# Performance work log

Hardware: AMD Instinct MI355X
Metric: run time of the kernel (lower is better)

The kernel has to match this reference:

```python
import jax, jax.numpy as jnp
import numpy as np

DIM = 512
HEADS = 8
LF, P = 32, 32
N = LF * P
LOC_DIM = 64  # loc_emd_dim == locf_dim == 64
SCALE = (DIM // HEADS) ** -0.5


def _position_matrix(boxes):
    # boxes: [N,4] x1y1x2y2 -> [N,N,4] relative geometry (relation-network style)
    x1, y1, x2, y2 = jnp.split(boxes, 4, axis=1)  # each [N,1]
    w = x2 - x1 + 1.0
    h = y2 - y1 + 1.0
    cx = 0.5 * (x1 + x2)
    cy = 0.5 * (y1 + y2)
    dx = jnp.log(jnp.maximum(jnp.abs((cx - cx.T) / w), 1e-3))
    dy = jnp.log(jnp.maximum(jnp.abs((cy - cy.T) / h), 1e-3))
    dw = jnp.log(w.T / w)
    dh = jnp.log(h.T / h)
    return jnp.stack([dx, dy, dw, dh], axis=-1)  # [N,N,4]


def _position_embedding(pos_mat, feat_dim=LOC_DIM, wave_length=1000.0):
    # pos_mat: [N,N,4] -> [N,N,feat_dim] sin/cos embedding
    nf = feat_dim // 8
    dim_mat = wave_length ** (jnp.arange(nf, dtype=jnp.float32) * (8.0 / feat_dim))  # [nf]
    div = pos_mat[..., None] * 100.0 / dim_mat  # [N,N,4,nf]
    emb = jnp.concatenate([jnp.sin(div), jnp.cos(div)], axis=-1)  # [N,N,4,2nf]
    return emb.reshape(pos_mat.shape[0], pos_mat.shape[1], feat_dim)


def setup_inputs() -> dict:
    key = jax.random.key(0)
    ks = jax.random.split(key, 8)
    x = jax.random.normal(ks[0], (1, N, DIM), jnp.float32)
    x_reg = jax.random.normal(ks[1], (1, N, DIM), jnp.float32)
    # valid boxes: x1y1x2y2 within a ~1000x600 frame
    cx = jax.random.uniform(ks[2], (LF, P, 1)) * 1000.0
    cy = jax.random.uniform(ks[3], (LF, P, 1)) * 600.0
    w = jax.random.uniform(ks[4], (LF, P, 1)) * 150.0 + 10.0
    h = jax.random.uniform(ks[5], (LF, P, 1)) * 150.0 + 10.0
    locs = jnp.concatenate([cx - w / 2, cy - h / 2, cx + w / 2, cy + h / 2], axis=-1)
    W_qkv = jax.random.normal(ks[6], (3 * DIM, DIM), jnp.float32) * 0.02
    W_loc = jax.random.normal(ks[7], (HEADS, LOC_DIM), jnp.float32) * 0.01  # 1x1 conv weight
    b_loc = jnp.zeros((HEADS,), jnp.float32)
    return {"x": x, "x_reg": x_reg, "locs": locs, "W_qkv": W_qkv, "W_loc": W_loc, "b_loc": b_loc}


def reference(x, x_reg, locs, W_qkv, W_loc, b_loc):
    B, n, C = x.shape
    boxes = locs.reshape(-1, 4)
    # location embedding -> 1x1 conv -> ReLU  (attn_lt: [H,N,N])
    pos_emb = _position_embedding(_position_matrix(boxes), LOC_DIM)  # [N,N,64]
    attn_lt = jax.nn.relu(jnp.einsum('nmf,hf->hnm', pos_emb, W_loc) + b_loc[:, None, None])
    # qkv projection (bias=False)
    qkv = (x @ W_qkv.T).reshape(B, n, 3, HEADS, C // HEADS)
    qkv = jnp.transpose(qkv, (2, 0, 3, 1, 4))  # [3,B,H,N,hd]
    q, k, v = qkv[0], qkv[1], qkv[2]
    attn = jnp.einsum('bhnd,bhmd->bhnm', q, k) * SCALE
    attn = attn + jnp.log(attn_lt + 1e-6)[None]  # loc_fuse_type == 'add'
    attn = jax.nn.softmax(attn, axis=-1)
    out = jnp.einsum('bhnm,bhmd->bhnd', attn, v)
    return jnp.transpose(out, (0, 2, 1, 3)).reshape(B, n, C)
```

## Files before the change

kernel.cpp:

```cpp
#include <hip/hip_runtime.h>
#include <hip/hip_bf16.h>


namespace {
constexpr int NN   = 1024;
constexpr int CDIM = 512;
constexpr int NH   = 8;
constexpr int HD   = 64;
constexpr int NOUT = 3 * CDIM;
constexpr int PROJ_BLOCKS = (NN / 64) * (NOUT / 64);
constexpr float QSCALE = 0.125f;

constexpr size_t QKBF_OFF_U16 = 0;
constexpr size_t VT_OFF_U16   = (size_t)2 * NH * NN * HD;
constexpr size_t XB_OFF_U16   = VT_OFF_U16 + (size_t)NH * HD * NN;
constexpr size_t WB_OFF_U16   = XB_OFF_U16 + (size_t)NN * CDIM;
constexpr size_t L_OFF_U16    = WB_OFF_U16 + (size_t)NOUT * CDIM;
constexpr size_t END_U16      = L_OFF_U16 + (size_t)NH * NN * NN;
constexpr size_t BF_OFF_F32   = END_U16 / 2;
constexpr size_t WR_OFF_F32   = BF_OFF_F32 + 6 * NN;
}

typedef __attribute__((ext_vector_type(8))) short short8v;
typedef __attribute__((ext_vector_type(4))) float f32x4;
typedef __attribute__((ext_vector_type(2))) float f32x2;

__device__ __forceinline__ unsigned short f2bf(float f) {
  union { float f; unsigned int u; } v; v.f = f;
  unsigned int u = v.u;
  u += 0x7fffu + ((u >> 16) & 1u);
  return (unsigned short)(u >> 16);
}
__device__ __forceinline__ float b2f(unsigned short u) {
  union { unsigned int u; float f; } v; v.u = ((unsigned int)u) << 16; return v.f;
}

__global__ __launch_bounds__(256) void k_cvt(const float* __restrict__ x,
                                             const float* __restrict__ wq,
                                             const float* __restrict__ locs,
                                             const float* __restrict__ wloc,
                                             const float* __restrict__ bloc,
                                             unsigned short* __restrict__ xb,
                                             unsigned short* __restrict__ wb,
                                             float* __restrict__ bf,
                                             float* __restrict__ wr) {
  constexpr int XTOT = NN * CDIM;
  constexpr int CVT_BLOCKS = 1280;
  int b = blockIdx.x;
  int tid = threadIdx.x;
  if (b < CVT_BLOCKS) {
    int idx = (b * 256 + tid) * 4;
    if (idx < XTOT) {
      float4 v = *reinterpret_cast<const float4*>(x + idx);
      ushort4 o;
      o.x = f2bf(v.x); o.y = f2bf(v.y); o.z = f2bf(v.z); o.w = f2bf(v.w);
      *reinterpret_cast<ushort4*>(xb + idx) = o;
    } else {
      int j = idx - XTOT;
      float4 v = *reinterpret_cast<const float4*>(wq + j);
      ushort4 o;
      o.x = f2bf(v.x); o.y = f2bf(v.y); o.z = f2bf(v.z); o.w = f2bf(v.w);
      *reinterpret_cast<ushort4*>(wb + j) = o;
    }
  } else {
    for (int i = tid; i < NN; i += 256) {
      float4 b4 = reinterpret_cast<const float4*>(locs)[i];
      float x1 = b4.x, y1 = b4.y, x2 = b4.z, y2 = b4.w;
      float w = x2 - x1 + 1.0f;
      float h = y2 - y1 + 1.0f;
      bf[0 * NN + i] = 0.5f * (x1 + x2);
      bf[1 * NN + i] = 0.5f * (y1 + y2);
      bf[2 * NN + i] = w;
      bf[3 * NN + i] = h;
      bf[4 * NN + i] = logf(w);
      bf[5 * NN + i] = logf(h);
    }
    for (int i = tid; i < 512; i += 256) {
      int hh = i & 7, c = (i >> 3) & 1, j = (i >> 4) & 3, t = i >> 6;
      wr[i] = wloc[hh * 64 + j * 16 + c * 8 + t];
    }
    if (tid < 8) wr[512 + tid] = bloc[tid];
  }
}

__global__ __launch_bounds__(256) void k_mid(const unsigned short* __restrict__ xb,
                                             const unsigned short* __restrict__ wb,
                                             unsigned short* __restrict__ qk_bf,
                                             unsigned short* __restrict__ vt,
                                             const float* __restrict__ bf,
                                             const float* __restrict__ wr,
                                             unsigned short* __restrict__ L) {
  __shared__ unsigned short A_lds[64][72];
  __shared__ unsigned short B_lds[64][72];
  int blk = blockIdx.x;
  int tid = threadIdx.x;

  if (blk >= PROJ_BLOCKS) {
    int blk2 = blk - PROJ_BLOCKS;
    int n = blk2 >> 2;
    int m = (blk2 & 3) * 256 + tid;
    const float* cx = bf;
    const float* cy = bf + NN;
    const float* bw = bf + 2 * NN;
    const float* bh = bf + 3 * NN;
    const float* lw = bf + 4 * NN;
    const float* lh = bf + 5 * NN;

    float cxn = cx[n], cyn = cy[n], wn = bw[n], hn = bh[n], lwn = lw[n], lhn = lh[n];
    float dx = __logf(fmaxf(fabsf((cxn - cx[m]) / wn), 1e-3f));
    float dy = __logf(fmaxf(fabsf((cyn - cy[m]) / hn), 1e-3f));
    float dw = lw[m] - lwn;
    float dh = lh[m] - lhn;
    float pos[4] = {dx, dy, dw, dh};

    const float ANG[8] = {100.0f, 42.169650342858224f, 17.78279410038923f,
                          7.498942093324559f, 3.1622776601683795f, 1.333521432163324f,
                          0.5623413251903491f, 0.23713737056616552f};

    f32x2 acc2[4] = {(f32x2){0.f, 0.f}, (f32x2){0.f, 0.f},
                     (f32x2){0.f, 0.f}, (f32x2){0.f, 0.f}};
#pragma unroll
    for (int t = 0; t < 8; ++t) {
#pragma unroll
      for (int j = 0; j < 4; ++j) {
        float s, c;
        __sincosf(pos[j] * ANG[t], &s, &c);
        const f32x2* wp2 = reinterpret_cast<const f32x2*>(wr + (t * 4 + j) * 16);
        f32x2 s2 = {s, s}, c2 = {c, c};
#pragma unroll
        for (int i = 0; i < 4; ++i) {
          acc2[i] += s2 * wp2[i] + c2 * wp2[4 + i];
        }
      }
    }
#pragma unroll
    for (int hh = 0; hh < 8; ++hh) {
      float v = fmaxf(acc2[hh >> 1][hh & 1] + wr[512 + hh], 0.0f);
      L[((size_t)hh * NN + n) * NN + m] = f2bf(v + 1e-6f);
    }
  } else {
    int t = blk;
    int n0 = (t & 15) * 64, i0 = (t >> 4) * 64;
    int w = tid >> 6, l = tid & 63, g = l >> 4, c = l & 15;
    int sr = tid >> 2;
    int sc = (tid & 3) * 16;

    f32x4 acc[4];
#pragma unroll
    for (int ct = 0; ct < 4; ++ct) acc[ct] = (f32x4){0.f, 0.f, 0.f, 0.f};

    for (int kt = 0; kt < CDIM; kt += 64) {
      const unsigned short* asrc = xb + (size_t)(n0 + sr) * CDIM + kt + sc;
      const unsigned short* bsrc = wb + (size_t)(i0 + sr) * CDIM + kt + sc;
      *reinterpret_cast<short8v*>(&A_lds[sr][sc])     = *reinterpret_cast<const short8v*>(asrc);
      *reinterpret_cast<short8v*>(&A_lds[sr][sc + 8]) = *reinterpret_cast<const short8v*>(asrc + 8);
      *reinterpret_cast<short8v*>(&B_lds[sr][sc])     = *reinterpret_cast<const short8v*>(bsrc);
      *reinterpret_cast<short8v*>(&B_lds[sr][sc + 8]) = *reinterpret_cast<const short8v*>(bsrc + 8);
      __syncthreads();
#pragma unroll
      for (int kks = 0; kks < 2; ++kks) {
        short8v a = *reinterpret_cast<const short8v*>(&A_lds[16 * w + c][kks * 32 + 8 * g]);
#pragma unroll
        for (int ct = 0; ct < 4; ++ct) {
          short8v b = *reinterpret_cast<const short8v*>(&B_lds[16 * ct + c][kks * 32 + 8 * g]);
          acc[ct] = __builtin_amdgcn_mfma_f32_16x16x32_bf16(a, b, acc[ct], 0, 0, 0);
        }
      }
      __syncthreads();
    }

    int s = i0 >> 9;
    int hh = (i0 >> 6) & 7;
    if (s < 2) {
      float scale = (s == 0) ? QSCALE : 1.0f;
      unsigned short* dst = qk_bf + ((size_t)(s * NH + hh) * NN) * HD;
#pragma unroll
      for (int ct = 0; ct < 4; ++ct)
#pragma unroll
        for (int r = 0; r < 4; ++r) {
          int n = n0 + 16 * w + 4 * g + r;
          dst[(size_t)n * HD + 16 * ct + c] = f2bf(acc[ct][r] * scale);
        }
    } else {
#pragma unroll
      for (int ct = 0; ct < 4; ++ct)
#pragma unroll
        for (int r = 0; r < 4; ++r) {
          A_lds[16 * w + 4 * g + r][16 * ct + c] = f2bf(acc[ct][r]);
        }
      __syncthreads();
      int d = tid >> 2;
      int nn0 = (tid & 3) * 16;
      unsigned short o[16];
#pragma unroll
      for (int nn = 0; nn < 16; ++nn) o[nn] = A_lds[nn0 + nn][d];
      unsigned short* dst = vt + ((size_t)hh * HD + d) * NN + n0 + nn0;
      *reinterpret_cast<short8v*>(dst)     = *reinterpret_cast<short8v*>(&o[0]);
      *reinterpret_cast<short8v*>(dst + 8) = *reinterpret_cast<short8v*>(&o[8]);
    }
  }
}

__global__ __launch_bounds__(512) void k_mha(const unsigned short* __restrict__ qk,
                                             const unsigned short* __restrict__ vt,
                                             const unsigned short* __restrict__ L,
                                             float* __restrict__ out) {
  __shared__ short8v smem16[3200];
  auto V = reinterpret_cast<unsigned short(*)[64][40]>(smem16);
  auto P = reinterpret_cast<unsigned short(*)[640]>(
      reinterpret_cast<char*>(smem16) + 40960);
  auto accs = reinterpret_cast<float(*)[16][68]>(smem16);
  auto mls = reinterpret_cast<float(*)[2][16]>(reinterpret_cast<char*>(smem16) + 34816);
  auto scw2 = reinterpret_cast<float(*)[16]>(reinterpret_cast<char*>(smem16) + 35840);
  auto rlf = reinterpret_cast<float*>(reinterpret_cast<char*>(smem16) + 36352);

  int tid = threadIdx.x;
  int w = tid >> 6;
  int l = tid & 63;
  int g = l >> 4;
  int c = l & 15;
  int h = blockIdx.y;
  int n0 = blockIdx.x * 16;

  const unsigned short* qb = qk + ((size_t)(0 * NH + h) * NN + n0) * HD;
  const unsigned short* kb = qk + ((size_t)(1 * NH + h) * NN) * HD;
  const unsigned short* vb = vt + (size_t)h * HD * NN;
  const unsigned short* Lb = L + ((size_t)h * NN + n0 + 4 * g) * NN;

  short8v a_lo = *reinterpret_cast<const short8v*>(qb + (size_t)c * HD + 8 * g);
  short8v a_hi = *reinterpret_cast<const short8v*>(qb + (size_t)c * HD + 32 + 8 * g);

  f32x4 acc[4];
#pragma unroll
  for (int ct = 0; ct < 4; ++ct) acc[ct] = (f32x4){0.f, 0.f, 0.f, 0.f};
  float m_run[4] = {-3.0e38f, -3.0e38f, -3.0e38f, -3.0e38f};
  float l_run[4] = {0.f, 0.f, 0.f, 0.f};

#pragma unroll
  for (int it = 0; it < 4; ++it) {
    int mt = w * 128 + it * 32;

#pragma unroll
    for (int p = 0; p < 4; ++p) {
      int d = p * 16 + (l >> 2);
      int key16 = (l & 3) * 8;
      *reinterpret_cast<short8v*>(&V[w][d][key16]) =
          *reinterpret_cast<const short8v*>(vb + (size_t)d * NN + mt + key16);
    }

    float t0[4], t1[4];
#pragma unroll
    for (int r = 0; r < 4; ++r) {
      t0[r] = b2f(Lb[(size_t)r * NN + mt + c]);
      t1[r] = b2f(Lb[(size_t)r * NN + mt + 16 + c]);
    }

    const unsigned short* k0p = kb + (size_t)(mt + c) * HD + 8 * g;
    const unsigned short* k1p = kb + (size_t)(mt + 16 + c) * HD + 8 * g;
    short8v b0_lo = *reinterpret_cast<const short8v*>(k0p);
    short8v b0_hi = *reinterpret_cast<const short8v*>(k0p + 32);
    short8v b1_lo = *reinterpret_cast<const short8v*>(k1p);
    short8v b1_hi = *reinterpret_cast<const short8v*>(k1p + 32);

    __builtin_amdgcn_s_setprio(1);
    f32x4 z = {0.f, 0.f, 0.f, 0.f};
    f32x4 s0 = __builtin_amdgcn_mfma_f32_16x16x32_bf16(a_lo, b0_lo, z, 0, 0, 0);
    s0 = __builtin_amdgcn_mfma_f32_16x16x32_bf16(a_hi, b0_hi, s0, 0, 0, 0);
    f32x4 s1 = __builtin_amdgcn_mfma_f32_16x16x32_bf16(a_lo, b1_lo, z, 0, 0, 0);
    s1 = __builtin_amdgcn_mfma_f32_16x16x32_bf16(a_hi, b1_hi, s1, 0, 0, 0);
    __builtin_amdgcn_s_setprio(0);

    float sc[4], p0[4], p1[4];
#pragma unroll
    for (int r = 0; r < 4; ++r) {
      float mx = fmaxf(s0[r], s1[r]);
      mx = fmaxf(mx, __shfl_xor(mx, 1));
      mx = fmaxf(mx, __shfl_xor(mx, 2));
      mx = fmaxf(mx, __shfl_xor(mx, 4));
      mx = fmaxf(mx, __shfl_xor(mx, 8));
      float m_new = fmaxf(m_run[r], mx);
      sc[r] = __expf(m_run[r] - m_new);
      p0[r] = t0[r] * __expf(s0[r] - m_new);
      p1[r] = t1[r] * __expf(s1[r] - m_new);
      l_run[r] = l_run[r] * sc[r] + (p0[r] + p1[r]);
      m_run[r] = m_new;
    }
#pragma unroll
    for (int ct = 0; ct < 4; ++ct)
#pragma unroll
      for (int r = 0; r < 4; ++r) acc[ct][r] *= sc[r];

#pragma unroll
    for (int r = 0; r < 4; ++r) {
      P[w][(4 * g + r) * 40 + c] = f2bf(p0[r]);
      P[w][(4 * g + r) * 40 + 16 + c] = f2bf(p1[r]);
    }
    __builtin_amdgcn_wave_barrier();

    short8v pa = *reinterpret_cast<const short8v*>(&P[w][c * 40 + 8 * g]);
    __builtin_amdgcn_s_setprio(1);
#pragma unroll
    for (int ct = 0; ct < 4; ++ct) {
      short8v vbf = *reinterpret_cast<const short8v*>(&V[w][ct * 16 + c][8 * g]);
      acc[ct] = __builtin_amdgcn_mfma_f32_16x16x32_bf16(pa, vbf, acc[ct], 0, 0, 0);
    }
    __builtin_amdgcn_s_setprio(0);
    __builtin_amdgcn_wave_barrier();
  }

#pragma unroll
  for (int r = 0; r < 4; ++r) {
    float ls = l_run[r];
    ls += __shfl_xor(ls, 1);
    ls += __shfl_xor(ls, 2);
    ls += __shfl_xor(ls, 4);
    ls += __shfl_xor(ls, 8);
    l_run[r] = ls;
  }

  __syncthreads();

  if (c == 0) {
#pragma unroll
    for (int r = 0; r < 4; ++r) {
      mls[w][0][4 * g + r] = m_run[r];
      mls[w][1][4 * g + r] = l_run[r];
    }
  }
#pragma unroll
  for (int ct = 0; ct < 4; ++ct)
#pragma unroll
    for (int r = 0; r < 4; ++r) accs[w][4 * g + r][ct * 16 + c] = acc[ct][r];
  __syncthreads();

  if (tid < 16) {
    int row = tid;
    float mfin = mls[0][0][row];
#pragma unroll
    for (int w2i = 1; w2i < 8; ++w2i) mfin = fmaxf(mfin, mls[w2i][0][row]);
    float lfin = 0.f;
#pragma unroll
    for (int w2i = 0; w2i < 8; ++w2i) {
      float scv = __expf(mls[w2i][0][row] - mfin);
      scw2[w2i][row] = scv;
      lfin += mls[w2i][1][row] * scv;
    }
    rlf[row] = 1.0f / lfin;
  }
  __syncthreads();

#pragma unroll
  for (int o = tid; o < 16 * 64; o += 512) {
    int row = o >> 6, col = o & 63;
    float val = 0.f;
#pragma unroll
    for (int w2i = 0; w2i < 8; ++w2i) {
      val += scw2[w2i][row] * accs[w2i][row][col];
    }
    out[(size_t)(n0 + row) * CDIM + h * HD + col] = val * rlf[row];
  }
}

extern "C" void kernel_launch(void* const* d_in, const int* in_sizes, int n_in,
                              void* d_out, int out_size, void* d_ws, size_t ws_size,
                              hipStream_t stream) {
  const float* x    = (const float*)d_in[0];
  const float* locs = (const float*)d_in[2];
  const float* wqkv = (const float*)d_in[3];
  const float* wloc = (const float*)d_in[4];
  const float* bloc = (const float*)d_in[5];
  float* out = (float*)d_out;
  float* ws = (float*)d_ws;
  unsigned short* ws_u16 = (unsigned short*)d_ws;

  unsigned short* qk_bf = ws_u16 + QKBF_OFF_U16;
  unsigned short* vt_bf = ws_u16 + VT_OFF_U16;
  unsigned short* xb    = ws_u16 + XB_OFF_U16;
  unsigned short* wb    = ws_u16 + WB_OFF_U16;
  unsigned short* L     = ws_u16 + L_OFF_U16;
  float* bf = ws + BF_OFF_F32;
  float* wr = ws + WR_OFF_F32;

  k_cvt<<<dim3(1281), dim3(256), 0, stream>>>(x, wqkv, locs, wloc, bloc, xb, wb, bf, wr);
  k_mid<<<dim3(PROJ_BLOCKS + 4096), dim3(256), 0, stream>>>(
      xb, wb, qk_bf, vt_bf, bf, wr, L);
  k_mha<<<dim3(NN / 16, NH), dim3(512), 0, stream>>>(qk_bf, vt_bf, L, out);
}
```

Baseline: 52.11 us.

## Compute location-embedding projection with bf16 MFMA instead of scalar FMAs

The position-embedding 64-to-8 projection moves from per-thread scalar FMAs to 16x16x32 bf16 MFMA instructions. Each lane now computes only two sincos pairs per geometry component rather than eight, and the W_loc weights are pre-packed as zero-padded bf16 in the convert kernel. This cuts transcendental and FMA work in the L-map stage. In exchange, half of the MFMA output rows are padding and are discarded, and the sin/cos features and weights are rounded to bf16, which lowers precision.

Measured after the change: 50.36 us (median of 2 runs). 3.4% less time.

```diff
diff --git a/kernel.cpp b/kernel.cpp
--- a/kernel.cpp
+++ b/kernel.cpp
@@ -19,11 +19,11 @@
 constexpr size_t END_U16      = L_OFF_U16 + (size_t)NH * NN * NN;
 constexpr size_t BF_OFF_F32   = END_U16 / 2;
 constexpr size_t WR_OFF_F32   = BF_OFF_F32 + 6 * NN;
+constexpr size_t W2_OFF_U16   = 2 * (WR_OFF_F32 + 528);
 }
 
 typedef __attribute__((ext_vector_type(8))) short short8v;
 typedef __attribute__((ext_vector_type(4))) float f32x4;
-typedef __attribute__((ext_vector_type(2))) float f32x2;
 
 __device__ __forceinline__ unsigned short f2bf(float f) {
   union { float f; unsigned int u; } v; v.f = f;
@@ -43,7 +43,8 @@
                                              unsigned short* __restrict__ xb,
                                              unsigned short* __restrict__ wb,
                                              float* __restrict__ bf,
-                                             float* __restrict__ wr) {
+                                             float* __restrict__ wr,
+                                             unsigned short* __restrict__ w2) {
   constexpr int XTOT = NN * CDIM;
   constexpr int CVT_BLOCKS = 1280;
   int b = blockIdx.x;
@@ -75,11 +76,13 @@
       bf[4 * NN + i] = logf(w);
       bf[5 * NN + i] = logf(h);
     }
-    for (int i = tid; i < 512; i += 256) {
-      int hh = i & 7, c = (i >> 3) & 1, j = (i >> 4) & 3, t = i >> 6;
-      wr[i] = wloc[hh * 64 + j * 16 + c * 8 + t];
-    }
     if (tid < 8) wr[512 + tid] = bloc[tid];
+    for (int i = tid; i < 16 * 64; i += 256) {
+      int hh = i >> 6, f = i & 63;
+      int sc = f & 1, tj = f >> 1, j = tj & 3, t = tj >> 2;
+      float v = (hh < 8) ? wloc[hh * 64 + j * 16 + sc * 8 + t] : 0.0f;
+      w2[i] = f2bf(v);
+    }
   }
 }
 
@@ -89,6 +92,7 @@
                                              unsigned short* __restrict__ vt,
                                              const float* __restrict__ bf,
                                              const float* __restrict__ wr,
+                                             const unsigned short* __restrict__ w2,
                                              unsigned short* __restrict__ L) {
   __shared__ unsigned short A_lds[64][72];
   __shared__ unsigned short B_lds[64][72];
@@ -98,45 +102,61 @@
   if (blk >= PROJ_BLOCKS) {
     int blk2 = blk - PROJ_BLOCKS;
     int n = blk2 >> 2;
-    int m = (blk2 & 3) * 256 + tid;
+    int m0 = (blk2 & 3) * 256;
+    int w = tid >> 6, l = tid & 63, g = l >> 4, c = l & 15;
+
     const float* cx = bf;
     const float* cy = bf + NN;
-    const float* bw = bf + 2 * NN;
-    const float* bh = bf + 3 * NN;
     const float* lw = bf + 4 * NN;
     const float* lh = bf + 5 * NN;
 
-    float cxn = cx[n], cyn = cy[n], wn = bw[n], hn = bh[n], lwn = lw[n], lhn = lh[n];
-    float dx = __logf(fmaxf(fabsf((cxn - cx[m]) / wn), 1e-3f));
-    float dy = __logf(fmaxf(fabsf((cyn - cy[m]) / hn), 1e-3f));
-    float dw = lw[m] - lwn;
-    float dh = lh[m] - lhn;
-    float pos[4] = {dx, dy, dw, dh};
-
-    const float ANG[8] = {100.0f, 42.169650342858224f, 17.78279410038923f,
-                          7.498942093324559f, 3.1622776601683795f, 1.333521432163324f,
-                          0.5623413251903491f, 0.23713737056616552f};
-
-    f32x2 acc2[4] = {(f32x2){0.f, 0.f}, (f32x2){0.f, 0.f},
-                     (f32x2){0.f, 0.f}, (f32x2){0.f, 0.f}};
-#pragma unroll
-    for (int t = 0; t < 8; ++t) {
+    float cxn = cx[n], cyn = cy[n];
+    float rwn = 1.0f / bf[2 * NN + n];
+    float rhn = 1.0f / bf[3 * NN + n];
+    float lwn = lw[n], lhn = lh[n];
+
+    float ang0 = 100.0f * exp2f(-1.2457230355894468f * (float)g);
+    float ang1 = ang0 * 0.031622776601683794f;
+
+    short8v aw_lo = *reinterpret_cast<const short8v*>(w2 + c * 64 + 8 * g);
+    short8v aw_hi = *reinterpret_cast<const short8v*>(w2 + c * 64 + 32 + 8 * g);
+    float br_[4];
+#pragma unroll
+    for (int r = 0; r < 4; ++r) br_[r] = wr[512 + ((4 * g + r) & 7)];
+
+#pragma unroll
+    for (int it = 0; it < 4; ++it) {
+      int m = m0 + w * 64 + it * 16 + c;
+      float dx = __logf(fmaxf(fabsf((cxn - cx[m]) * rwn), 1e-3f));
+      float dy = __logf(fmaxf(fabsf((cyn - cy[m]) * rhn), 1e-3f));
+      float dwv = lw[m] - lwn;
+      float dhv = lh[m] - lhn;
+      float pos[4] = {dx, dy, dwv, dhv};
+
+      union BU { unsigned int u[4]; short8v v; } b0, b1;
 #pragma unroll
       for (int j = 0; j < 4; ++j) {
-        float s, c;
-        __sincosf(pos[j] * ANG[t], &s, &c);
-        const f32x2* wp2 = reinterpret_cast<const f32x2*>(wr + (t * 4 + j) * 16);
-        f32x2 s2 = {s, s}, c2 = {c, c};
-#pragma unroll
-        for (int i = 0; i < 4; ++i) {
-          acc2[i] += s2 * wp2[i] + c2 * wp2[4 + i];
+        float s0v, c0v, s1v, c1v;
+        __sincosf(pos[j] * ang0, &s0v, &c0v);
+        __sincosf(pos[j] * ang1, &s1v, &c1v);
+        union { __hip_bfloat162 h; unsigned int u; } cv0, cv1;
+        cv0.h = __float22bfloat162_rn(make_float2(s0v, c0v));
+        cv1.h = __float22bfloat162_rn(make_float2(s1v, c1v));
+        b0.u[j] = cv0.u;
+        b1.u[j] = cv1.u;
+      }
+
+      f32x4 z = {0.f, 0.f, 0.f, 0.f};
+      f32x4 acc4 = __builtin_amdgcn_mfma_f32_16x16x32_bf16(aw_lo, b0.v, z, 0, 0, 0);
+      acc4 = __builtin_amdgcn_mfma_f32_16x16x32_bf16(aw_hi, b1.v, acc4, 0, 0, 0);
+
+      if (g < 2) {
+#pragma unroll
+        for (int r = 0; r < 4; ++r) {
+          float v = fmaxf(acc4[r] + br_[r], 0.0f) + 1e-6f;
+          L[((size_t)(4 * g + r) * NN + n) * NN + m] = f2bf(v);
         }
       }
-    }
-#pragma unroll
-    for (int hh = 0; hh < 8; ++hh) {
-      float v = fmaxf(acc2[hh >> 1][hh & 1] + wr[512 + hh], 0.0f);
-      L[((size_t)hh * NN + n) * NN + m] = f2bf(v + 1e-6f);
     }
   } else {
     int t = blk;
@@ -378,11 +398,12 @@
   unsigned short* xb    = ws_u16 + XB_OFF_U16;
   unsigned short* wb    = ws_u16 + WB_OFF_U16;
   unsigned short* L     = ws_u16 + L_OFF_U16;
+  unsigned short* w2    = ws_u16 + W2_OFF_U16;
   float* bf = ws + BF_OFF_F32;
   float* wr = ws + WR_OFF_F32;
 
-  k_cvt<<<dim3(1281), dim3(256), 0, stream>>>(x, wqkv, locs, wloc, bloc, xb, wb, bf, wr);
+  k_cvt<<<dim3(1281), dim3(256), 0, stream>>>(x, wqkv, locs, wloc, bloc, xb, wb, bf, wr, w2);
   k_mid<<<dim3(PROJ_BLOCKS + 4096), dim3(256), 0, stream>>>(
-      xb, wb, qk_bf, vt_bf, bf, wr, L);
+      xb, wb, qk_bf, vt_bf, bf, wr, w2, L);
   k_mha<<<dim3(NN / 16, NH), dim3(512), 0, stream>>>(qk_bf, vt_bf, L, out);
 }
```
